# Performance work log

Hardware: AMD Instinct MI355X
Metric: run time of the kernel (lower is better)

The kernel has to match this reference:

```python
import jax, jax.numpy as jnp
import numpy as np

FACTOR = 0.1   # init_kwargs factor
EPS = 1e-7
B, C, H, W = 256, 3, 224, 224


def setup_inputs() -> dict:
    key = jax.random.key(0)
    k1, k2, k3 = jax.random.split(key, 3)
    x = jax.random.normal(k1, (B, C, H, W), dtype=jnp.float32)
    shift_fy = jax.random.uniform(k2, (B,), dtype=jnp.float32)  # maps to torch.rand(1)
    shift_fx = jax.random.uniform(k3, (B,), dtype=jnp.float32)
    return {"x": x, "shift_fy": shift_fy, "shift_fx": shift_fx}


def _shift_axis(img, shift, axis, size):
    # Equivalent to torch in-place slice copy + zero-fill:
    #   shift>0: img[..., :size-shift] = img[..., shift:]; img[..., size-shift:] = 0
    #   shift<0: img[..., -shift:]   = img[..., :shift];  img[..., :-shift]   = 0
    # == roll by -shift, then zero positions j where j+shift is out of [0, size)
    idx = jnp.arange(size)
    rolled = jnp.roll(img, -shift, axis=axis)
    mask = (idx + shift >= 0) & (idx + shift < size)
    shp = [1, 1, 1]
    shp[axis] = size
    return rolled * mask.reshape(shp).astype(img.dtype)


def _per_image(img, fy, fx):
    # img: [C, H, W]
    h, w = img.shape[1], img.shape[2]
    # int(shift_factor * size) truncates toward zero -> jnp.trunc
    sy = jnp.trunc((fy * 2.0 - 1.0) * FACTOR * h).astype(jnp.int32)
    sx = jnp.trunc((fx * 2.0 - 1.0) * FACTOR * w).astype(jnp.int32)
    img = _shift_axis(img, sy, 1, h)
    img = _shift_axis(img, sx, 2, w)
    # standardize with unbiased std (torch.std default, ddof=1)
    n = img.size
    mean = jnp.mean(img)
    var = jnp.sum(jnp.square(img - mean)) / (n - 1)
    img = (img - mean) / (jnp.sqrt(var) + EPS)
    # min-max normalize
    mn = jnp.min(img)
    mx = jnp.max(img)
    return (img - mn) / (mx - mn)


def reference(x, shift_fy, shift_fx):
    # fully vectorized over the batch (original uses a Python per-image loop)
    return jax.vmap(_per_image)(x, shift_fy, shift_fx)
```

## Files before the change

kernel.cpp:

```cpp
#include <hip/hip_runtime.h>
#include <math.h>


constexpr int kC = 3, kH = 224, kW = 224;
constexpr int kCHW  = kC * kH * kW;
constexpr int kROWS = kC * kH;
constexpr int kQPR  = kW / 4;
constexpr int TB    = 1024;
constexpr int WVB   = TB / 64;
constexpr int RPW   = kROWS / WVB;

typedef float f32x4 __attribute__((ext_vector_type(4)));

template <int R>
__device__ __forceinline__ void phase2_rows(const float* __restrict__ xb,
                                            float* __restrict__ ob,
                                            int sy, int sx, float inv,
                                            float zoff, int wv, int lane)
{
    if (lane >= kQPR) return;
    const int i0   = lane * 4;
    const int base = i0 + sx - R;
    int qa = base;     qa = qa < 0 ? 0 : qa; qa = qa > kW - 4 ? kW - 4 : qa;
    int qb = base + 4; qb = qb < 0 ? 0 : qb; qb = qb > kW - 4 ? kW - 4 : qb;

    float cm[4];
    #pragma unroll
    for (int k = 0; k < 4; ++k)
        cm[k] = ((unsigned)(i0 + k + sx) < (unsigned)kW) ? 1.0f : 0.0f;
    const f32x4 zq = {zoff, zoff, zoff, zoff};

    #pragma unroll 3
    for (int t = 0; t < RPW; ++t) {
        const int rr = wv + t * WVB;
        const int j  = rr % kH;
        const int jj = j + sy;
        float* __restrict__ dst = ob + rr * kW + i0;
        if ((unsigned)jj < (unsigned)kH) {
            const float* __restrict__ src = xb + (rr - j + jj) * kW;
            const f32x4 av = *(const f32x4*)(src + qa);
            const f32x4 bv = *(const f32x4*)(src + qb);
            f32x4 o;
            #pragma unroll
            for (int k = 0; k < 4; ++k) {
                const float sel = (k + R < 4) ? av[k + R] : bv[k + R - 4];
                o[k] = fmaf(sel * cm[k], inv, zoff);
            }
            *(f32x4*)dst = o;
        } else {
            *(f32x4*)dst = zq;
        }
    }
}

__global__ __launch_bounds__(TB) void shift_norm(
    const float* __restrict__ x, const float* __restrict__ sfy,
    const float* __restrict__ sfx, float* __restrict__ out)
{
    const int img = blockIdx.x;
    const float* __restrict__ xb = x + (size_t)img * kCHW;
    float* __restrict__ ob = out + (size_t)img * kCHW;

    float ty = sfy[img] * 2.0f - 1.0f; ty *= 0.1f; ty *= (float)kH;
    const int sy = (int)truncf(ty);
    float tx = sfx[img] * 2.0f - 1.0f; tx *= 0.1f; tx *= (float)kW;
    const int sx = (int)truncf(tx);

    const int rlo = sy > 0 ? sy : 0;
    const int rhi = kH + (sy < 0 ? sy : 0);
    const int clo = sx > 0 ? sx : 0;
    const int chi = kW + (sx < 0 ? sx : 0);

    const int tid  = threadIdx.x;
    const int lane = tid & 63;
    const int wv   = __builtin_amdgcn_readfirstlane(tid >> 6);

    const bool hasfill = (sy != 0) | (sx != 0);
    float vmin = hasfill ? 0.0f : INFINITY;
    float vmax = hasfill ? 0.0f : -INFINITY;

    if (lane < kQPR) {
        const int i0 = lane * 4;
        float cm[4];
        #pragma unroll
        for (int k = 0; k < 4; ++k)
            cm[k] = ((i0 + k) >= clo && (i0 + k) < chi) ? 1.0f : 0.0f;

        #pragma unroll 6
        for (int t = 0; t < RPW; ++t) {
            const int rr = wv + t * WVB;
            const int j  = rr % kH;
            if (j >= rlo && j < rhi) {
                const f32x4 v = *(const f32x4*)(xb + rr * kW + i0);
                #pragma unroll
                for (int k = 0; k < 4; ++k) {
                    const float val = v[k] * cm[k];
                    vmin = fminf(vmin, val);
                    vmax = fmaxf(vmax, val);
                }
            }
        }
    }

    #pragma unroll
    for (int off = 32; off > 0; off >>= 1) {
        vmin = fminf(vmin, __shfl_down(vmin, off));
        vmax = fmaxf(vmax, __shfl_down(vmax, off));
    }
    __shared__ float smin[WVB], smax[WVB];
    __shared__ float s_mn, s_inv;
    if (lane == 0) { smin[tid >> 6] = vmin; smax[tid >> 6] = vmax; }
    __syncthreads();
    if (tid == 0) {
        float mn = smin[0], mx = smax[0];
        #pragma unroll
        for (int w = 1; w < WVB; ++w) {
            mn = fminf(mn, smin[w]);
            mx = fmaxf(mx, smax[w]);
        }
        s_mn  = mn;
        s_inv = 1.0f / (mx - mn);
    }
    __syncthreads();
    const float mn   = s_mn;
    const float inv  = s_inv;
    const float zoff = (0.0f - mn) * inv;

    switch (sx & 3) {
        case 0: phase2_rows<0>(xb, ob, sy, sx, inv, zoff, wv, lane); break;
        case 1: phase2_rows<1>(xb, ob, sy, sx, inv, zoff, wv, lane); break;
        case 2: phase2_rows<2>(xb, ob, sy, sx, inv, zoff, wv, lane); break;
        default: phase2_rows<3>(xb, ob, sy, sx, inv, zoff, wv, lane); break;
    }
}

extern "C" void kernel_launch(void* const* d_in, const int* in_sizes, int n_in,
                              void* d_out, int out_size, void* d_ws, size_t ws_size,
                              hipStream_t stream) {
    const float* x  = (const float*)d_in[0];
    const float* fy = (const float*)d_in[1];
    const float* fx = (const float*)d_in[2];
    float* out = (float*)d_out;
    const int B = in_sizes[1];
    shift_norm<<<B, TB, 0, stream>>>(x, fy, fx, out);
}
```

Measured before the change: 299.1 us.

## Split min/max reduction and write pass into producer/consumer blocks with flags

Separates the per-image min/max reduction and the normalized write into different workgroups. Producer blocks each reduce two images and publish min/max through global flags, while consumer blocks spin-wait on the flag and then write. The block size is also halved to 512 threads. The goal is to overlap the read-heavy reduction of some images with the write phase of others and raise occupancy. In exchange it adds a memset, spin-waiting that can deadlock if consumers fill the device before producers are scheduled, and a second read of x from a different block that may no longer hit cache.

```diff
diff --git a/kernel.cpp b/kernel.cpp
--- a/kernel.cpp
+++ b/kernel.cpp
@@ -6,11 +6,64 @@
 constexpr int kCHW  = kC * kH * kW;
 constexpr int kROWS = kC * kH;
 constexpr int kQPR  = kW / 4;
-constexpr int TB    = 1024;
+constexpr int TB    = 512;
 constexpr int WVB   = TB / 64;
 constexpr int RPW   = kROWS / WVB;
 
 typedef float f32x4 __attribute__((ext_vector_type(4)));
+
+__device__ __forceinline__ void shifts_for(const float* __restrict__ sfy,
+                                           const float* __restrict__ sfx,
+                                           int img, int& sy, int& sx)
+{
+    float ty = sfy[img] * 2.0f - 1.0f; ty *= 0.1f; ty *= (float)kH;
+    sy = (int)truncf(ty);
+    float tx = sfx[img] * 2.0f - 1.0f; tx *= 0.1f; tx *= (float)kW;
+    sx = (int)truncf(tx);
+}
+
+__device__ __forceinline__ void minmax_image(const float* __restrict__ xb,
+                                             int sy, int sx, int lane, int wv,
+                                             float& omn, float& omx)
+{
+    const int rlo = sy > 0 ? sy : 0;
+    const int rhi = kH + (sy < 0 ? sy : 0);
+    const int clo = sx > 0 ? sx : 0;
+    const int chi = kW + (sx < 0 ? sx : 0);
+
+    const bool hasfill = (sy != 0) | (sx != 0);
+    float vmin = hasfill ? 0.0f : INFINITY;
+    float vmax = hasfill ? 0.0f : -INFINITY;
+
+    if (lane < kQPR) {
+        const int i0 = lane * 4;
+        float cm[4];
+        #pragma unroll
+        for (int k = 0; k < 4; ++k)
+            cm[k] = ((i0 + k) >= clo && (i0 + k) < chi) ? 1.0f : 0.0f;
+
+        #pragma unroll 6
+        for (int t = 0; t < RPW; ++t) {
+            const int rr = wv + t * WVB;
+            const int j  = rr % kH;
+            if (j >= rlo && j < rhi) {
+                const f32x4 v = *(const f32x4*)(xb + rr * kW + i0);
+                #pragma unroll
+                for (int k = 0; k < 4; ++k) {
+                    const float val = v[k] * cm[k];
+                    vmin = fminf(vmin, val);
+                    vmax = fmaxf(vmax, val);
+                }
+            }
+        }
+    }
+    #pragma unroll
+    for (int off = 32; off > 0; off >>= 1) {
+        vmin = fminf(vmin, __shfl_down(vmin, off));
+        vmax = fmaxf(vmax, __shfl_down(vmax, off));
+    }
+    omn = vmin; omx = vmax;
+}
 
 template <int R>
 __device__ __forceinline__ void phase2_rows(const float* __restrict__ xb,
@@ -53,84 +106,79 @@
     }
 }
 
-__global__ __launch_bounds__(TB) void shift_norm(
+__global__ __launch_bounds__(TB) void shift_pipe(
     const float* __restrict__ x, const float* __restrict__ sfy,
-    const float* __restrict__ sfx, float* __restrict__ out)
-{
-    const int img = blockIdx.x;
-    const float* __restrict__ xb = x + (size_t)img * kCHW;
-    float* __restrict__ ob = out + (size_t)img * kCHW;
-
-    float ty = sfy[img] * 2.0f - 1.0f; ty *= 0.1f; ty *= (float)kH;
-    const int sy = (int)truncf(ty);
-    float tx = sfx[img] * 2.0f - 1.0f; tx *= 0.1f; tx *= (float)kW;
-    const int sx = (int)truncf(tx);
-
-    const int rlo = sy > 0 ? sy : 0;
-    const int rhi = kH + (sy < 0 ? sy : 0);
-    const int clo = sx > 0 ? sx : 0;
-    const int chi = kW + (sx < 0 ? sx : 0);
-
+    const float* __restrict__ sfx, float* __restrict__ out,
+    unsigned* __restrict__ flag, unsigned* __restrict__ mnb,
+    unsigned* __restrict__ mxb, int B, int HALF)
+{
+    const int bid  = blockIdx.x;
     const int tid  = threadIdx.x;
     const int lane = tid & 63;
     const int wv   = __builtin_amdgcn_readfirstlane(tid >> 6);
 
-    const bool hasfill = (sy != 0) | (sx != 0);
-    float vmin = hasfill ? 0.0f : INFINITY;
-    float vmax = hasfill ? 0.0f : -INFINITY;
-
-    if (lane < kQPR) {
-        const int i0 = lane * 4;
-        float cm[4];
-        #pragma unroll
-        for (int k = 0; k < 4; ++k)
-            cm[k] = ((i0 + k) >= clo && (i0 + k) < chi) ? 1.0f : 0.0f;
-
-        #pragma unroll 6
-        for (int t = 0; t < RPW; ++t) {
-            const int rr = wv + t * WVB;
-            const int j  = rr % kH;
-            if (j >= rlo && j < rhi) {
-                const f32x4 v = *(const f32x4*)(xb + rr * kW + i0);
+    __shared__ float smin[WVB], smax[WVB];
+    __shared__ float s_a, s_b;
+
+    if (bid < HALF) {
+        #pragma unroll 1
+        for (int c = 0; c < 2; ++c) {
+            const int img = bid + c * HALF;
+            if (img >= B) break;
+            const float* __restrict__ xb = x + (size_t)img * kCHW;
+            int sy, sx; shifts_for(sfy, sfx, img, sy, sx);
+
+            float vmin, vmax;
+            minmax_image(xb, sy, sx, lane, wv, vmin, vmax);
+            if (lane == 0) { smin[wv] = vmin; smax[wv] = vmax; }
+            __syncthreads();
+            if (tid == 0) {
+                float mn = smin[0], mx = smax[0];
                 #pragma unroll
-                for (int k = 0; k < 4; ++k) {
-                    const float val = v[k] * cm[k];
-                    vmin = fminf(vmin, val);
-                    vmax = fmaxf(vmax, val);
+                for (int w = 1; w < WVB; ++w) {
+                    mn = fminf(mn, smin[w]);
+                    mx = fmaxf(mx, smax[w]);
                 }
+                __hip_atomic_store(&mnb[img], __float_as_uint(mn),
+                                   __ATOMIC_RELAXED, __HIP_MEMORY_SCOPE_AGENT);
+                __hip_atomic_store(&mxb[img], __float_as_uint(mx),
+                                   __ATOMIC_RELAXED, __HIP_MEMORY_SCOPE_AGENT);
+                __hip_atomic_store(&flag[img], 1u,
+                                   __ATOMIC_RELEASE, __HIP_MEMORY_SCOPE_AGENT);
             }
-        }
-    }
-
-    #pragma unroll
-    for (int off = 32; off > 0; off >>= 1) {
-        vmin = fminf(vmin, __shfl_down(vmin, off));
-        vmax = fmaxf(vmax, __shfl_down(vmax, off));
-    }
-    __shared__ float smin[WVB], smax[WVB];
-    __shared__ float s_mn, s_inv;
-    if (lane == 0) { smin[tid >> 6] = vmin; smax[tid >> 6] = vmax; }
-    __syncthreads();
-    if (tid == 0) {
-        float mn = smin[0], mx = smax[0];
-        #pragma unroll
-        for (int w = 1; w < WVB; ++w) {
-            mn = fminf(mn, smin[w]);
-            mx = fmaxf(mx, smax[w]);
-        }
-        s_mn  = mn;
-        s_inv = 1.0f / (mx - mn);
-    }
-    __syncthreads();
-    const float mn   = s_mn;
-    const float inv  = s_inv;
-    const float zoff = (0.0f - mn) * inv;
-
-    switch (sx & 3) {
-        case 0: phase2_rows<0>(xb, ob, sy, sx, inv, zoff, wv, lane); break;
-        case 1: phase2_rows<1>(xb, ob, sy, sx, inv, zoff, wv, lane); break;
-        case 2: phase2_rows<2>(xb, ob, sy, sx, inv, zoff, wv, lane); break;
-        default: phase2_rows<3>(xb, ob, sy, sx, inv, zoff, wv, lane); break;
+            __syncthreads();
+        }
+    } else {
+        const int img = bid - HALF;
+        if (img >= B) return;
+        const float* __restrict__ xb = x + (size_t)img * kCHW;
+        float* __restrict__ ob = out + (size_t)img * kCHW;
+        int sy, sx; shifts_for(sfy, sfx, img, sy, sx);
+
+        if (tid == 0) {
+            while (__hip_atomic_load(&flag[img], __ATOMIC_ACQUIRE,
+                                     __HIP_MEMORY_SCOPE_AGENT) == 0u)
+                __builtin_amdgcn_s_sleep(2);
+            const float mn = __uint_as_float(
+                __hip_atomic_load(&mnb[img], __ATOMIC_RELAXED,
+                                  __HIP_MEMORY_SCOPE_AGENT));
+            const float mx = __uint_as_float(
+                __hip_atomic_load(&mxb[img], __ATOMIC_RELAXED,
+                                  __HIP_MEMORY_SCOPE_AGENT));
+            s_a = mn;
+            s_b = 1.0f / (mx - mn);
+        }
+        __syncthreads();
+        const float mn   = s_a;
+        const float inv  = s_b;
+        const float zoff = (0.0f - mn) * inv;
+
+        switch (sx & 3) {
+            case 0: phase2_rows<0>(xb, ob, sy, sx, inv, zoff, wv, lane); break;
+            case 1: phase2_rows<1>(xb, ob, sy, sx, inv, zoff, wv, lane); break;
+            case 2: phase2_rows<2>(xb, ob, sy, sx, inv, zoff, wv, lane); break;
+            default: phase2_rows<3>(xb, ob, sy, sx, inv, zoff, wv, lane); break;
+        }
     }
 }
 
@@ -142,5 +190,12 @@
     const float* fx = (const float*)d_in[2];
     float* out = (float*)d_out;
     const int B = in_sizes[1];
-    shift_norm<<<B, TB, 0, stream>>>(x, fy, fx, out);
-}
+    const int HALF = (B + 1) / 2;
+
+    unsigned* flag = (unsigned*)d_ws;
+    unsigned* mnb  = flag + B;
+    unsigned* mxb  = mnb + B;
+    hipMemsetAsync(d_ws, 0, (size_t)B * sizeof(unsigned), stream);
+
+    shift_pipe<<<HALF + B, TB, 0, stream>>>(x, fy, fx, out, flag, mnb, mxb, B, HALF);
+}
```

After: 491.1 us. 64.2% more time.
